# Kernel tuning notes

Measured on AMD Instinct MI355X. Metric: run time of the kernel, lower is better.

The kernel has to match this reference:

```python
import jax, jax.numpy as jnp
import numpy as np
from jax import lax

B, N, S, C_IN, C_OUT = 4, 16384, 4096, 256, 256


def setup_inputs() -> dict:
    key = jax.random.key(0)
    k1, k2, k3, k4 = jax.random.split(key, 4)
    xyz1 = jax.random.normal(k1, (B, 3, N), dtype=jnp.float32)
    xyz2 = jax.random.normal(k2, (B, 3, S), dtype=jnp.float32)
    points2 = jax.random.normal(k3, (B, C_IN, S), dtype=jnp.float32)
    W = jax.random.normal(k4, (C_OUT, C_IN), dtype=jnp.float32) * (1.0 / np.sqrt(C_IN))
    b = jnp.zeros((C_OUT,), dtype=jnp.float32)
    return {"xyz1": xyz1, "xyz2": xyz2, "points2": points2, "W": W, "b": b}


def reference(xyz1, xyz2, points2, W, b):
    # channel-first -> channel-last
    p1 = jnp.transpose(xyz1, (0, 2, 1))        # [B, N, 3]
    p2 = jnp.transpose(xyz2, (0, 2, 1))        # [B, S, 3]
    f2 = jnp.transpose(points2, (0, 2, 1))     # [B, S, C]
    Bn, Nn, _ = p1.shape
    Cn = f2.shape[-1]
    # squared pairwise distances [B, N, S]
    d = (-2.0 * jnp.einsum('bnc,bsc->bns', p1, p2)
         + jnp.sum(p1 * p1, axis=-1)[:, :, None]
         + jnp.sum(p2 * p2, axis=-1)[:, None, :])
    # 3 nearest neighbors (smallest distances) -- equivalent to sort + slice :3
    neg_d3, idx = lax.top_k(-d, 3)             # [B, N, 3]
    d3 = -neg_d3
    recip = 1.0 / (d3 + 1e-8)
    weight = recip / jnp.sum(recip, axis=-1, keepdims=True)   # [B, N, 3]
    # gather neighbor features: [B, N, 3, C]
    gathered = jnp.take_along_axis(
        f2, idx.reshape(Bn, Nn * 3)[..., None], axis=1
    ).reshape(Bn, Nn, 3, Cn)
    interp = jnp.sum(gathered * weight[..., None], axis=2)    # [B, N, C]
    # Conv1d(kernel=1) == per-point linear: [B, C_out, N]
    out = jnp.einsum('bnc,oc->bon', interp, W) + b[None, :, None]
    return out
```

## Files before the change

kernel.cpp:

```cpp
#include <hip/hip_runtime.h>

#define BB 4
#define NN 16384
#define SS 4096
#define CIN 256
#define COUT 256

#define SC 8
#define SCS (SS / SC)
#define SUBS 16
#define SUBL 256
#define KNNB ((NN / 512) * SC * BB)
#define GEMMB ((COUT / 64) * (SS / 64) * BB)
#define RSLVB (BB * (NN / 64))

typedef float v2f __attribute__((ext_vector_type(2)));
typedef float v4f __attribute__((ext_vector_type(4)));

__device__ __forceinline__ unsigned short f2bf(float f) {
    unsigned u = __float_as_uint(f);
    u += 0x7FFF + ((u >> 16) & 1);
    return (unsigned short)(u >> 16);
}
__device__ __forceinline__ float bf2f(unsigned short h) {
    return __uint_as_float((unsigned)h << 16);
}

__device__ __forceinline__ void insert_vi(float e, int gi,
                                          float& k0, float& k1, float& k2,
                                          int& i0, int& i1, int& i2) {
    bool c0 = e < k0, c1 = e < k1, c2 = e < k2;
    float n0 = fminf(e, k0);
    float n1 = __builtin_amdgcn_fmed3f(e, k0, k1);
    float n2 = __builtin_amdgcn_fmed3f(e, k1, k2);
    int t1 = c0 ? i0 : gi;
    int t2 = c1 ? i1 : gi;
    i0 = c0 ? gi : i0;
    i1 = c1 ? t1 : i1;
    i2 = c2 ? t2 : i2;
    k0 = n0; k1 = n1; k2 = n2;
}

#define E2_FROM(p_xy, p_zw, XX, YY, ZZ, e2)                                    \
    do {                                                                       \
        asm("v_pk_fma_f32 %0, %1, %2, %3 op_sel:[0,0,1] op_sel_hi:[0,1,1]"     \
            : "=v"(e2) : "v"(p_zw), "v"(ZZ), "v"(p_zw));                       \
        asm("v_pk_fma_f32 %0, %1, %2, %0 op_sel:[1,0,0] op_sel_hi:[1,1,1]"     \
            : "+v"(e2) : "v"(p_xy), "v"(YY));                                  \
        asm("v_pk_fma_f32 %0, %1, %2, %0 op_sel:[0,0,0] op_sel_hi:[0,1,1]"     \
            : "+v"(e2) : "v"(p_xy), "v"(XX));                                  \
    } while (0)

#define PK_LO(acc, ap, bw)                                                     \
    asm("v_pk_fma_f32 %0, %1, %2, %0 op_sel:[0,0,0] op_sel_hi:[0,1,1]"         \
        : "+v"(acc) : "v"(ap), "v"(bw))
#define PK_HI(acc, ap, bw)                                                     \
    asm("v_pk_fma_f32 %0, %1, %2, %0 op_sel:[1,0,0] op_sel_hi:[1,1,1]"         \
        : "+v"(acc) : "v"(ap), "v"(bw))

__device__ __forceinline__ void knn_phase(int id, int t, float* smem,
                                          const float* __restrict__ xyz1,
                                          const float* __restrict__ xyz2,
                                          float* __restrict__ pv,
                                          float4* __restrict__ cand4) {
    int nb = id & 31;
    int ch = (id >> 5) & 7;
    int b  = id >> 8;
    int s0 = ch * SCS;

    float4* smv = (float4*)smem;
    const float* x2 = xyz2 + (size_t)b * 3 * SS;
    for (int i = t; i < SCS; i += 256) {
        float px = x2[s0 + i];
        float py = x2[SS + s0 + i];
        float pz = x2[2 * SS + s0 + i];
        float4 p4 = make_float4(px, py, pz, fmaf(px, px, fmaf(py, py, pz * pz)));
        smv[i] = p4;
        if (nb == 0) cand4[(size_t)b * SS + s0 + i] = p4;
    }
    __syncthreads();

    int n0  = nb * 512 + t;
    int n1q = n0 + 256;
    const float* xb = xyz1 + (size_t)b * 3 * NN;
    float ax = xb[n0],  ay = xb[NN + n0],  az = xb[2 * NN + n0];
    float bx = xb[n1q], by = xb[NN + n1q], bz = xb[2 * NN + n1q];
    v2f XX = {-2.0f * ax, -2.0f * bx};
    v2f YY = {-2.0f * ay, -2.0f * by};
    v2f ZZ = {-2.0f * az, -2.0f * bz};

#pragma unroll
    for (int half = 0; half < 2; ++half) {
        float A0 = 1e30f, A1 = 1e30f, A2 = 1e30f;
        float B0 = 1e30f, B1 = 1e30f, B2 = 1e30f;
        int sb = half * SUBL;
#pragma unroll 8
        for (int s = sb; s < sb + SUBL; ++s) {
            v4f p = *(const v4f*)(smem + 4 * s);
            v2f pxy = __builtin_shufflevector(p, p, 0, 1);
            v2f pzw = __builtin_shufflevector(p, p, 2, 3);
            v2f e2;
            E2_FROM(pxy, pzw, XX, YY, ZZ, e2);
            float nA1 = __builtin_amdgcn_fmed3f(e2.x, A0, A1);
            float nA2 = __builtin_amdgcn_fmed3f(e2.x, A1, A2);
            A0 = fminf(A0, e2.x); A1 = nA1; A2 = nA2;
            float nB1 = __builtin_amdgcn_fmed3f(e2.y, B0, B1);
            float nB2 = __builtin_amdgcn_fmed3f(e2.y, B1, B2);
            B0 = fminf(B0, e2.y); B1 = nB1; B2 = nB2;
        }
        int sub = ch * 2 + half;
        size_t base = (size_t)(sub * BB + b) * 3;
        pv[(base + 0) * NN + n0]  = A0;
        pv[(base + 1) * NN + n0]  = A1;
        pv[(base + 2) * NN + n0]  = A2;
        pv[(base + 0) * NN + n1q] = B0;
        pv[(base + 1) * NN + n1q] = B1;
        pv[(base + 2) * NN + n1q] = B2;
    }
}

__device__ __forceinline__ void gemm_phase(int g, int t, float* smem,
                                           const float* __restrict__ P,
                                           const float* __restrict__ W,
                                           const float* __restrict__ bias,
                                           unsigned short* __restrict__ Gh) {
    int o0 = (g & 3) * 64;
    int s0 = ((g >> 2) & 63) * 64;
    int b  = g >> 8;
    float* sP = smem;
    float* sW = smem + 1024;
    int i = t & 15;
    int j = t >> 4;

    v2f acc2[4][2];
#pragma unroll
    for (int p = 0; p < 4; ++p) {
        acc2[p][0] = (v2f){0.f, 0.f};
        acc2[p][1] = (v2f){0.f, 0.f};
    }

    const float* Pb = P + (size_t)b * CIN * SS;

    for (int c0 = 0; c0 < CIN; c0 += 16) {
        __syncthreads();
        {
            int col = t & 63;
            int r0r = t >> 6;
#pragma unroll
            for (int r = 0; r < 4; ++r) {
                int row = r0r + r * 4;
                sP[row * 64 + col] = Pb[(size_t)(c0 + row) * SS + s0 + col];
            }
        }
        {
            int cc = t & 15;
            int obase = t >> 4;
#pragma unroll
            for (int r = 0; r < 4; ++r) {
                int oo = obase + 16 * r;
                sW[cc * 68 + oo] = W[(size_t)(o0 + oo) * CIN + c0 + cc];
            }
        }
        __syncthreads();

#pragma unroll
        for (int cc = 0; cc < 16; ++cc) {
            v4f a  = *(const v4f*)&sP[cc * 64 + i * 4];
            v4f bv = *(const v4f*)&sW[cc * 68 + j * 4];
            v2f a01 = __builtin_shufflevector(a, a, 0, 1);
            v2f a23 = __builtin_shufflevector(a, a, 2, 3);
            v2f b01 = __builtin_shufflevector(bv, bv, 0, 1);
            v2f b23 = __builtin_shufflevector(bv, bv, 2, 3);
            PK_LO(acc2[0][0], a01, b01); PK_LO(acc2[0][1], a01, b23);
            PK_HI(acc2[1][0], a01, b01); PK_HI(acc2[1][1], a01, b23);
            PK_LO(acc2[2][0], a23, b01); PK_LO(acc2[2][1], a23, b23);
            PK_HI(acc2[3][0], a23, b01); PK_HI(acc2[3][1], a23, b23);
        }
    }

    float b0 = bias[o0 + j * 4 + 0];
    float b1 = bias[o0 + j * 4 + 1];
    float b2 = bias[o0 + j * 4 + 2];
    float b3 = bias[o0 + j * 4 + 3];
#pragma unroll
    for (int p = 0; p < 4; ++p) {
        ushort4 v;
        v.x = f2bf(acc2[p][0].x + b0);
        v.y = f2bf(acc2[p][0].y + b1);
        v.z = f2bf(acc2[p][1].x + b2);
        v.w = f2bf(acc2[p][1].y + b3);
        size_t off = ((size_t)b * SS + s0 + i * 4 + p) * COUT + o0 + j * 4;
        *(ushort4*)&Gh[off] = v;
    }
}

__global__ __launch_bounds__(256) void k_fused(const float* __restrict__ xyz1,
                                               const float* __restrict__ xyz2,
                                               const float* __restrict__ P,
                                               const float* __restrict__ W,
                                               const float* __restrict__ bias,
                                               unsigned short* __restrict__ Gh,
                                               float* __restrict__ pv,
                                               float4* __restrict__ cand4) {
    __shared__ float smem[2112];
    int bid = blockIdx.x;
    int t   = threadIdx.x;

    if (bid < KNNB) {
        knn_phase(bid, t, smem, xyz1, xyz2, pv, cand4);
    } else {
        gemm_phase(bid - KNNB, t, smem, P, W, bias, Gh);
    }
}

__global__ __launch_bounds__(256) void k_resolve(const float* __restrict__ pv,
                                                 const float* __restrict__ xyz1,
                                                 const float4* __restrict__ cand4,
                                                 float4* __restrict__ wi4,
                                                 int4* __restrict__ gi4) {
    __shared__ float sv[4][64][3];
    __shared__ int   si[4][64][3];
    int bid  = blockIdx.x;
    int b    = bid >> 8;
    int nblk = bid & 255;
    int t    = threadIdx.x;
    int k    = t >> 6;
    int q    = t & 63;
    int n    = nblk * 64 + q;

    float a0s[SUBS];
    float v0 = 1e30f, v1 = 1e30f, v2v = 1e30f;
#pragma unroll
    for (int sub = 0; sub < SUBS; ++sub) {
        size_t base = (size_t)(sub * BB + b) * 3;
#pragma unroll
        for (int j = 0; j < 3; ++j) {
            float a = pv[(base + j) * NN + n];
            if (j == 0) a0s[sub] = a;
            float t1 = __builtin_amdgcn_fmed3f(a, v0, v1);
            float t2 = __builtin_amdgcn_fmed3f(a, v1, v2v);
            v0 = fminf(v0, a); v1 = t1; v2v = t2;
        }
    }

    int lk = 0, cnt = 0;
#pragma unroll
    for (int sub = 0; sub < SUBS; ++sub) {
        bool w = (a0s[sub] <= v2v);
        if (w && cnt == k) lk = sub;
        cnt += w ? 1 : 0;
    }

    float k0 = 1e30f, k1 = 1e30f, k2 = 1e30f;
    int   i0 = 0,     i1 = 0,     i2 = 0;
    bool ovf = (cnt > 4);
    bool act = !ovf && (k < cnt);
    const float* xb = xyz1 + (size_t)b * 3 * NN;
    float qx = xb[n], qy = xb[NN + n], qz = xb[2 * NN + n];
    float xm2 = -2.0f * qx, ym2 = -2.0f * qy, zm2 = -2.0f * qz;
    const float4* cb = cand4 + (size_t)b * SS;

    if (act) {
        int sb = lk * SUBL;
#pragma unroll 4
        for (int s = 0; s < SUBL; ++s) {
            float4 p = cb[sb + s];
            float e = fmaf(p.x, xm2, fmaf(p.y, ym2, fmaf(p.z, zm2, p.w)));
            insert_vi(e, sb + s, k0, k1, k2, i0, i1, i2);
        }
    }
    if (__any(ovf && k == 0)) {
        if (ovf && k == 0) {
            for (int s = 0; s < SS; ++s) {
                float4 p = cb[s];
                float e = fmaf(p.x, xm2, fmaf(p.y, ym2, fmaf(p.z, zm2, p.w)));
                insert_vi(e, s, k0, k1, k2, i0, i1, i2);
            }
        }
    }

    sv[k][q][0] = k0; sv[k][q][1] = k1; sv[k][q][2] = k2;
    si[k][q][0] = i0; si[k][q][1] = i1; si[k][q][2] = i2;
    __syncthreads();

    if (t < 64) {
        float K0 = 1e30f, K1 = 1e30f, K2 = 1e30f;
        int   I0 = 0,     I1 = 0,     I2 = 0;
#pragma unroll
        for (int kk = 0; kk < 4; ++kk)
#pragma unroll
            for (int j = 0; j < 3; ++j)
                insert_vi(sv[kk][t][j], si[kk][t][j], K0, K1, K2, I0, I1, I2);

        int nn = nblk * 64 + t;
        float ax = xb[nn], ay = xb[NN + nn], az = xb[2 * NN + nn];
        float nrm = fmaf(ax, ax, fmaf(ay, ay, az * az));
        float d0 = K0 + nrm, d1 = K1 + nrm, d2 = K2 + nrm;
        float r0 = 1.0f / (d0 + 1e-8f);
        float r1 = 1.0f / (d1 + 1e-8f);
        float r2 = 1.0f / (d2 + 1e-8f);
        float inv = 1.0f / (r0 + r1 + r2);
        size_t oq = (size_t)b * NN + nn;
        wi4[oq] = make_float4(r0 * inv, r1 * inv, r2 * inv, 0.f);
        gi4[oq] = make_int4(I0, I1, I2, 0);
    }
}

__global__ __launch_bounds__(256) void k_out(const unsigned short* __restrict__ Gh,
                                             const float4* __restrict__ wi4,
                                             const int4* __restrict__ gi4,
                                             float* __restrict__ out) {
    __shared__ float  tile[64 * 68];
    __shared__ float4 swv[64];
    __shared__ int4   siv[64];
    int bid  = blockIdx.x;
    int x    = bid & 7;
    int b    = x >> 1;
    int local = (bid >> 3) + (x & 1) * 512;
    int nb   = local & 255;
    int oc   = local >> 8;
    int n0   = nb * 64;
    int o0   = oc * 64;
    int t    = threadIdx.x;
    int wave = t >> 6;
    int lane = t & 63;
    int qg   = lane >> 4;
    int c16  = lane & 15;

    if (t < 64) {
        size_t q = (size_t)b * NN + n0 + t;
        swv[t] = wi4[q];
        siv[t] = gi4[q];
    }
    __syncthreads();

    const unsigned short* Gb = Gh + (size_t)b * SS * COUT;

#pragma unroll
    for (int pass = 0; pass < 4; ++pass) {
        int q = pass * 16 + wave * 4 + qg;
        float4 wv = swv[q];
        int4   iv = siv[q];
        int co = o0 + c16 * 4;
        ushort4 a0 = *(const ushort4*)(Gb + (size_t)iv.x * COUT + co);
        ushort4 a1 = *(const ushort4*)(Gb + (size_t)iv.y * COUT + co);
        ushort4 a2 = *(const ushort4*)(Gb + (size_t)iv.z * COUT + co);
        float4 v;
        v.x = fmaf(wv.x, bf2f(a0.x), fmaf(wv.y, bf2f(a1.x), wv.z * bf2f(a2.x)));
        v.y = fmaf(wv.x, bf2f(a0.y), fmaf(wv.y, bf2f(a1.y), wv.z * bf2f(a2.y)));
        v.z = fmaf(wv.x, bf2f(a0.z), fmaf(wv.y, bf2f(a1.z), wv.z * bf2f(a2.z)));
        v.w = fmaf(wv.x, bf2f(a0.w), fmaf(wv.y, bf2f(a1.w), wv.z * bf2f(a2.w)));
        *(float4*)&tile[q * 68 + c16 * 4] = v;
    }
    __syncthreads();

    float* obase = out + ((size_t)b * COUT + o0) * NN + n0 + lane;
#pragma unroll
    for (int g = 0; g < 4; ++g) {
        int c = wave * 16 + g * 4;
        float4 v = *(const float4*)&tile[lane * 68 + c];
        obase[(size_t)(c + 0) * NN] = v.x;
        obase[(size_t)(c + 1) * NN] = v.y;
        obase[(size_t)(c + 2) * NN] = v.z;
        obase[(size_t)(c + 3) * NN] = v.w;
    }
}

extern "C" void kernel_launch(void* const* d_in, const int* in_sizes, int n_in,
                              void* d_out, int out_size, void* d_ws, size_t ws_size,
                              hipStream_t stream) {
    const float* xyz1    = (const float*)d_in[0];
    const float* xyz2    = (const float*)d_in[1];
    const float* points2 = (const float*)d_in[2];
    const float* W       = (const float*)d_in[3];
    const float* bias    = (const float*)d_in[4];
    float* out = (float*)d_out;

    char* ws = (char*)d_ws;
    float*          pv  = (float*)(ws);
    unsigned short* Gh  = (unsigned short*)(ws + 12582912);
    float4*         wi4 = (float4*)(ws + 20971520);
    int4*           gi4 = (int4*)(ws + 22020096);
    float4* cand4 = (float4*)((char*)d_out + 66846720);

    k_fused<<<dim3(KNNB + GEMMB), 256, 0, stream>>>(xyz1, xyz2, points2, W, bias,
                                                    Gh, pv, cand4);
    k_resolve<<<dim3(RSLVB), 256, 0, stream>>>(pv, xyz1, cand4, wi4, gi4);
    k_out<<<dim3(4096), 256, 0, stream>>>(Gh, wi4, gi4, out);
}
```

Measured before the change: 241.9 us.

## Resolve each query with one wavefront using shuffle reductions and ballot compaction

The resolve kernel now assigns one whole wavefront per query point instead of one thread per query with four candidate slices. Partial minima are merged with xor-shuffle top-3 reductions, and qualifying sub-chunks are scanned cooperatively across lanes. Survivors are compacted through ballot and mbcnt into shared memory, then merged with a lexicographic tie-break. This removes serial per-thread 256-element scans and the overflow full scan by a single lane. In exchange it launches 16x more blocks, leaves most lanes idle during the final merge, and keeps a serial fallback path when the compacted list overflows.

Result: faster. 208.8 us (-13.7%).

```diff
diff --git a/kernel.cpp b/kernel.cpp
--- a/kernel.cpp
+++ b/kernel.cpp
@@ -12,7 +12,7 @@
 #define SUBL 256
 #define KNNB ((NN / 512) * SC * BB)
 #define GEMMB ((COUT / 64) * (SS / 64) * BB)
-#define RSLVB (BB * (NN / 64))
+#define RSLVB (BB * NN / 4)
 
 typedef float v2f __attribute__((ext_vector_type(2)));
 typedef float v4f __attribute__((ext_vector_type(4)));
@@ -24,6 +24,12 @@
 }
 __device__ __forceinline__ float bf2f(unsigned short h) {
     return __uint_as_float((unsigned)h << 16);
+}
+
+__device__ __forceinline__ void ins_v(float e, float& a, float& b, float& c) {
+    float n1 = __builtin_amdgcn_fmed3f(e, a, b);
+    float n2 = __builtin_amdgcn_fmed3f(e, b, c);
+    a = fminf(a, e); b = n1; c = n2;
 }
 
 __device__ __forceinline__ void insert_vi(float e, int gi,
@@ -39,6 +45,28 @@
     i1 = c1 ? t1 : i1;
     i2 = c2 ? t2 : i2;
     k0 = n0; k1 = n1; k2 = n2;
+}
+
+__device__ __forceinline__ void ins_lex(float e, int gi,
+                                        float& k0, float& k1, float& k2,
+                                        int& i0, int& i1, int& i2) {
+    bool c0 = (e < k0) || (e == k0 && gi < i0);
+    bool c1 = (e < k1) || (e == k1 && gi < i1);
+    bool c2 = (e < k2) || (e == k2 && gi < i2);
+    float n0 = fminf(e, k0);
+    float n1 = __builtin_amdgcn_fmed3f(e, k0, k1);
+    float n2 = __builtin_amdgcn_fmed3f(e, k1, k2);
+    int t1 = c0 ? i0 : gi;
+    int t2 = c1 ? i1 : gi;
+    i0 = c0 ? gi : i0;
+    i1 = c1 ? t1 : i1;
+    i2 = c2 ? t2 : i2;
+    k0 = n0; k1 = n1; k2 = n2;
+}
+
+__device__ __forceinline__ int ltc(unsigned long long m) {
+    return __builtin_amdgcn_mbcnt_hi(
+        (unsigned)(m >> 32), __builtin_amdgcn_mbcnt_lo((unsigned)m, 0));
 }
 
 #define E2_FROM(p_xy, p_zw, XX, YY, ZZ, e2)                                    \
@@ -218,89 +246,90 @@
                                                  const float4* __restrict__ cand4,
                                                  float4* __restrict__ wi4,
                                                  int4* __restrict__ gi4) {
-    __shared__ float sv[4][64][3];
-    __shared__ int   si[4][64][3];
-    int bid  = blockIdx.x;
-    int b    = bid >> 8;
-    int nblk = bid & 255;
-    int t    = threadIdx.x;
-    int k    = t >> 6;
-    int q    = t & 63;
-    int n    = nblk * 64 + q;
-
-    float a0s[SUBS];
-    float v0 = 1e30f, v1 = 1e30f, v2v = 1e30f;
-#pragma unroll
-    for (int sub = 0; sub < SUBS; ++sub) {
-        size_t base = (size_t)(sub * BB + b) * 3;
-#pragma unroll
-        for (int j = 0; j < 3; ++j) {
-            float a = pv[(base + j) * NN + n];
-            if (j == 0) a0s[sub] = a;
-            float t1 = __builtin_amdgcn_fmed3f(a, v0, v1);
-            float t2 = __builtin_amdgcn_fmed3f(a, v1, v2v);
-            v0 = fminf(v0, a); v1 = t1; v2v = t2;
-        }
-    }
-
-    int lk = 0, cnt = 0;
-#pragma unroll
-    for (int sub = 0; sub < SUBS; ++sub) {
-        bool w = (a0s[sub] <= v2v);
-        if (w && cnt == k) lk = sub;
-        cnt += w ? 1 : 0;
-    }
+    __shared__ uint2 sl[4][16];
+    int t   = threadIdx.x;
+    int wid = t >> 6;
+    int l   = t & 63;
+    int g   = blockIdx.x * 4 + wid;
+    int b   = g >> 14;
+    int n   = g & (NN - 1);
+
+    float ov = 1e30f;
+    if (l < 48)
+        ov = pv[(size_t)(((l & 15) * BB + b) * 3 + (l >> 4)) * NN + n];
+    float m0 = ov, m1 = 1e30f, m2 = 1e30f;
+#pragma unroll
+    for (int xm = 1; xm < 64; xm <<= 1) {
+        float s0 = __shfl_xor(m0, xm);
+        float s1 = __shfl_xor(m1, xm);
+        float s2 = __shfl_xor(m2, xm);
+        ins_v(s0, m0, m1, m2);
+        ins_v(s1, m0, m1, m2);
+        ins_v(s2, m0, m1, m2);
+    }
+
+    unsigned mm = (unsigned)__ballot((l < 16) && (ov <= m2)) & 0xFFFFu;
+
+    const float* xb = xyz1 + (size_t)b * 3 * NN;
+    float qx = xb[n], qy = xb[NN + n], qz = xb[2 * NN + n];
+    float xm2c = -2.0f * qx, ym2c = -2.0f * qy, zm2c = -2.0f * qz;
+    const float4* cb = cand4 + (size_t)b * SS;
 
     float k0 = 1e30f, k1 = 1e30f, k2 = 1e30f;
     int   i0 = 0,     i1 = 0,     i2 = 0;
-    bool ovf = (cnt > 4);
-    bool act = !ovf && (k < cnt);
-    const float* xb = xyz1 + (size_t)b * 3 * NN;
-    float qx = xb[n], qy = xb[NN + n], qz = xb[2 * NN + n];
-    float xm2 = -2.0f * qx, ym2 = -2.0f * qy, zm2 = -2.0f * qz;
-    const float4* cb = cand4 + (size_t)b * SS;
-
-    if (act) {
-        int sb = lk * SUBL;
-#pragma unroll 4
-        for (int s = 0; s < SUBL; ++s) {
-            float4 p = cb[sb + s];
-            float e = fmaf(p.x, xm2, fmaf(p.y, ym2, fmaf(p.z, zm2, p.w)));
-            insert_vi(e, sb + s, k0, k1, k2, i0, i1, i2);
-        }
-    }
-    if (__any(ovf && k == 0)) {
-        if (ovf && k == 0) {
-            for (int s = 0; s < SS; ++s) {
-                float4 p = cb[s];
-                float e = fmaf(p.x, xm2, fmaf(p.y, ym2, fmaf(p.z, zm2, p.w)));
-                insert_vi(e, s, k0, k1, k2, i0, i1, i2);
+    unsigned msc = mm;
+    while (msc) {
+        int sub = __builtin_ctz(msc); msc &= msc - 1;
+        int sb = sub * SUBL;
+#pragma unroll
+        for (int r = 0; r < 4; ++r) {
+            int gi = sb + r * 64 + l;
+            float4 p = cb[gi];
+            float e = fmaf(p.x, xm2c, fmaf(p.y, ym2c, fmaf(p.z, zm2c, p.w)));
+            insert_vi(e, gi, k0, k1, k2, i0, i1, i2);
+        }
+    }
+
+    unsigned long long b0 = __ballot(k0 <= m2);
+    unsigned long long b1 = __ballot(k1 <= m2);
+    unsigned long long b2 = __ballot(k2 <= m2);
+    int p0 = __popcll(b0), p1 = __popcll(b1);
+    int cnt3 = p0 + p1 + __popcll(b2);
+    if (cnt3 <= 16) {
+        if (k0 <= m2) sl[wid][ltc(b0)]           = make_uint2(__float_as_uint(k0), (unsigned)i0);
+        if (k1 <= m2) sl[wid][p0 + ltc(b1)]      = make_uint2(__float_as_uint(k1), (unsigned)i1);
+        if (k2 <= m2) sl[wid][p0 + p1 + ltc(b2)] = make_uint2(__float_as_uint(k2), (unsigned)i2);
+    }
+    __syncthreads();
+
+    float K0 = 1e30f, K1 = 1e30f, K2 = 1e30f;
+    int   I0 = 0,     I1 = 0,     I2 = 0;
+    if (cnt3 <= 16) {
+        for (int j = 0; j < cnt3; ++j) {
+            uint2 u = sl[wid][j];
+            ins_lex(__uint_as_float(u.x), (int)u.y, K0, K1, K2, I0, I1, I2);
+        }
+    } else {
+        unsigned mf = mm;
+        while (mf) {
+            int sub = __builtin_ctz(mf); mf &= mf - 1;
+            int sb = sub * SUBL;
+            for (int s = 0; s < SUBL; ++s) {
+                float4 p = cb[sb + s];
+                float e = fmaf(p.x, xm2c, fmaf(p.y, ym2c, fmaf(p.z, zm2c, p.w)));
+                ins_lex(e, sb + s, K0, K1, K2, I0, I1, I2);
             }
         }
     }
 
-    sv[k][q][0] = k0; sv[k][q][1] = k1; sv[k][q][2] = k2;
-    si[k][q][0] = i0; si[k][q][1] = i1; si[k][q][2] = i2;
-    __syncthreads();
-
-    if (t < 64) {
-        float K0 = 1e30f, K1 = 1e30f, K2 = 1e30f;
-        int   I0 = 0,     I1 = 0,     I2 = 0;
-#pragma unroll
-        for (int kk = 0; kk < 4; ++kk)
-#pragma unroll
-            for (int j = 0; j < 3; ++j)
-                insert_vi(sv[kk][t][j], si[kk][t][j], K0, K1, K2, I0, I1, I2);
-
-        int nn = nblk * 64 + t;
-        float ax = xb[nn], ay = xb[NN + nn], az = xb[2 * NN + nn];
-        float nrm = fmaf(ax, ax, fmaf(ay, ay, az * az));
+    if (l == 0) {
+        float nrm = fmaf(qx, qx, fmaf(qy, qy, qz * qz));
         float d0 = K0 + nrm, d1 = K1 + nrm, d2 = K2 + nrm;
         float r0 = 1.0f / (d0 + 1e-8f);
         float r1 = 1.0f / (d1 + 1e-8f);
         float r2 = 1.0f / (d2 + 1e-8f);
         float inv = 1.0f / (r0 + r1 + r2);
-        size_t oq = (size_t)b * NN + nn;
+        size_t oq = (size_t)b * NN + n;
         wi4[oq] = make_float4(r0 * inv, r1 * inv, r2 * inv, 0.f);
         gi4[oq] = make_int4(I0, I1, I2, 0);
     }
```
